# Performance work log

Measured on AMD Instinct MI355X. Metric: run time of the kernel, lower is better.

## Reference

```python
import jax, jax.numpy as jnp
from jax import lax
import numpy as np
import math

H = 768
INNER = 1152  # int(1.5*768), divisible by num_heads
NH = 8
DH = INNER // NH
K = 4
B = 2
S = 2048


def setup_inputs() -> dict:
    key = jax.random.key(0)
    ks = jax.random.split(key, 12)
    sc = 0.02
    inp = {
        'x': jax.random.normal(ks[0], (B, S, H), dtype=jnp.float32),
        'W_up': jax.random.normal(ks[1], (H, 2 * INNER), dtype=jnp.float32) * sc,
        'conv_w': jax.random.normal(ks[2], (INNER, 1, K), dtype=jnp.float32) * sc,  # depthwise OIW
        'conv_b': jnp.zeros((INNER,), dtype=jnp.float32),
        'Wq': jax.random.normal(ks[3], (INNER, INNER), dtype=jnp.float32) * sc,
        'Wk': jax.random.normal(ks[4], (INNER, INNER), dtype=jnp.float32) * sc,
        'Wv': jax.random.normal(ks[5], (INNER, INNER), dtype=jnp.float32) * sc,
        'Wi': jnp.zeros((3 * INNER, NH), dtype=jnp.float32),
        'bi': jax.random.normal(ks[6], (NH,), dtype=jnp.float32) * 0.1,
        'Wf': jnp.zeros((3 * INNER, NH), dtype=jnp.float32),
        'bf': jnp.linspace(3.0, 6.0, NH, dtype=jnp.float32),
        'norm_w': jnp.ones((INNER,), dtype=jnp.float32),
        'skip': jnp.ones((), dtype=jnp.float32),
        'W_down': jax.random.normal(ks[7], (INNER, H), dtype=jnp.float32) * sc,
    }
    return inp


def _multihead_layernorm(h, norm_w, eps=1e-5):
    # per-head layernorm, no bias, computed in fp32
    b, s, d = h.shape
    hh = h.reshape(b, s, NH, DH).astype(jnp.float32)
    mean = hh.mean(axis=-1, keepdims=True)
    var = ((hh - mean) ** 2).mean(axis=-1, keepdims=True)
    hn = (hh - mean) / jnp.sqrt(var + eps)
    return hn.reshape(b, s, d).astype(h.dtype) * norm_w


def _mlstm_cell(q, k, v, Wi, bi, Wf, bf, norm_w):
    b, s, d = q.shape
    eps = 1e-6
    qkv_cat = jnp.concatenate([q, k, v], axis=-1)          # (B,S,3*INNER)
    ig = qkv_cat @ Wi + bi                                  # (B,S,NH)
    fg = qkv_cat @ Wf + bf                                  # (B,S,NH)
    # to (B,NH,S,DH)
    qh = q.reshape(b, s, NH, DH).transpose(0, 2, 1, 3)
    kh = k.reshape(b, s, NH, DH).transpose(0, 2, 1, 3)
    vh = v.reshape(b, s, NH, DH).transpose(0, 2, 1, 3)
    ig = ig.transpose(0, 2, 1)                              # (B,NH,S)
    fg = fg.transpose(0, 2, 1)                              # (B,NH,S)

    log_f = jax.nn.log_sigmoid(fg)                          # (B,NH,S)
    lf_cs = jnp.concatenate([jnp.zeros((b, NH, 1), log_f.dtype),
                             jnp.cumsum(log_f, axis=-1)], axis=-1)  # (B,NH,S+1)
    # entry (i,j) = sum log f_{j+1..i}
    log_fg_mat = lf_cs[:, :, 1:, None] - lf_cs[:, :, None, 1:]      # (B,NH,S,S)
    ltr = jnp.tril(jnp.ones((s, s), dtype=bool))
    log_fg_mat = jnp.where(ltr, log_fg_mat, -jnp.inf)
    log_D = log_fg_mat + ig[:, :, None, :]                  # add igate along columns
    max_log_D = lax.stop_gradient(jnp.max(log_D, axis=-1, keepdims=True))
    D = jnp.exp(log_D - max_log_D)                          # (B,NH,S,S)

    qk = jnp.einsum('bhsd,bhtd->bhst', qh, kh / math.sqrt(DH))
    C = qk * D
    normalizer = jnp.maximum(jnp.abs(C.sum(axis=-1, keepdims=True)),
                             jnp.exp(-max_log_D)) + eps
    h = jnp.einsum('bhst,bhtd->bhsd', C / normalizer, vh)
    h = h.transpose(0, 2, 1, 3).reshape(b, s, d)
    return _multihead_layernorm(h, norm_w)


def reference(x, W_up, conv_w, conv_b, Wq, Wk, Wv, Wi, bi, Wf, bf, norm_w, skip, W_down):
    xz = x @ W_up                                           # (B,S,2*INNER)
    x_mlstm, z = jnp.split(xz, 2, axis=-1)
    # causal depthwise conv1d
    xc = x_mlstm.transpose(0, 2, 1)                         # NCW
    xc = jnp.pad(xc, ((0, 0), (0, 0), (K - 1, 0)))
    xc = lax.conv_general_dilated(xc, conv_w, (1,), 'VALID',
                                  dimension_numbers=('NCW', 'OIW', 'NCW'),
                                  feature_group_count=INNER)
    xc = (xc + conv_b[None, :, None]).transpose(0, 2, 1)    # (B,S,INNER)
    x_conv = jax.nn.silu(xc)
    q = x_conv @ Wq
    k = x_conv @ Wk
    v = x_mlstm @ Wv
    h = _mlstm_cell(q, k, v, Wi, bi, Wf, bf, norm_w)
    h = h + skip * x_conv
    h = h * jax.nn.silu(z)
    return h @ W_down
```

## Files before the change

### kernel.cpp

```cpp
#include <hip/hip_runtime.h>
#include <hip/hip_bf16.h>
#include <math.h>

#define HDIM   768
#define INNER  1152
#define NHEADS 8
#define DHEAD  144
#define SEQ    2048
#define BATCH  2
#define TOKENS (BATCH*SEQ)

using bf16x8 = __attribute__((ext_vector_type(8))) short;
using u16x8  = __attribute__((ext_vector_type(8))) unsigned short;
using f32x4  = __attribute__((ext_vector_type(4))) float;

__device__ __forceinline__ float silu_f(float x) { return x / (1.f + expf(-x)); }

__device__ __forceinline__ unsigned short f2bf(float f) {
    unsigned u = __float_as_uint(f);
    unsigned r = (u + 0x7fffu + ((u >> 16) & 1u)) >> 16;
    return (unsigned short)r;
}
__device__ __forceinline__ float bf2f(unsigned short s) {
    return __uint_as_float(((unsigned)s) << 16);
}

#define MF(a, b, c) __builtin_amdgcn_mfma_f32_16x16x32_bf16(a, b, c, 0, 0, 0)

__global__ __launch_bounds__(256) void convert_act(
    const float* __restrict__ X, int ldx, int Kd, unsigned short* __restrict__ Y) {
    int t = blockIdx.x * 256 + threadIdx.x;
    int kc = Kd >> 3;
    int k8 = t % kc;
    int row = t / kc;
    int k = k8 * 8;
    const float* src = X + (size_t)row * ldx + k;
    float4 v0 = *(const float4*)src;
    float4 v1 = *(const float4*)(src + 4);
    float a[8] = {v0.x, v0.y, v0.z, v0.w, v1.x, v1.y, v1.z, v1.w};
    u16x8 hi, lo;
#pragma unroll
    for (int j = 0; j < 8; ++j) {
        unsigned short h = f2bf(a[j]);
        hi[j] = h;
        lo[j] = f2bf(a[j] - bf2f(h));
    }
    int rb = row >> 7, r = row & 127, kb = k >> 5, c = k & 31;
    int KB = Kd >> 5;
    size_t base = ((size_t)(rb * KB + kb) * 2) * 4096;
    *(u16x8*)&Y[base + r * 32 + c] = hi;
    *(u16x8*)&Y[base + 4096 + r * 32 + c] = lo;
}

__global__ __launch_bounds__(256) void convert_wgt(
    const float* __restrict__ W, int N, int Kd, unsigned short* __restrict__ Y) {
    __shared__ float ls[32][133];
    const int tid = threadIdx.x;
    const int cb = blockIdx.x, kb = blockIdx.y;
    for (int i = tid; i < 4096; i += 256) {
        int kk = i >> 7, n = i & 127;
        ls[kk][n] = W[(size_t)(kb * 32 + kk) * N + cb * 128 + n];
    }
    __syncthreads();
    int KB = Kd >> 5;
    unsigned short* dst = Y + ((size_t)(cb * KB + kb) * 2) * 4096;
#pragma unroll
    for (int g = 0; g < 2; ++g) {
        int u = g * 256 + tid;
        int j = u >> 2, kk0 = (u & 3) * 8;
        u16x8 hi, lo;
#pragma unroll
        for (int e = 0; e < 8; ++e) {
            float a = ls[kk0 + e][j];
            unsigned short h = f2bf(a);
            hi[e] = h;
            lo[e] = f2bf(a - bf2f(h));
        }
        *(u16x8*)&dst[j * 32 + kk0] = hi;
        *(u16x8*)&dst[4096 + j * 32 + kk0] = lo;
    }
}

__global__ __launch_bounds__(256) void gemm_bf16x3(
    const unsigned short* __restrict__ At, const unsigned short* __restrict__ Bt,
    float* __restrict__ C, int N, int KB) {
    __shared__ unsigned short lsA[2][128][32];
    __shared__ unsigned short lsB[2][128][32];
    const int tid = threadIdx.x;
    const int w = tid >> 6, lane = tid & 63;
    const int wr = w >> 1, wc = w & 1;
    const int bx = blockIdx.x, by = blockIdx.y;

    const unsigned short* ga0 = At + ((size_t)by * KB) * 8192;
    const unsigned short* gb0 = Bt + ((size_t)bx * KB) * 8192;
    unsigned short* lsAf = &lsA[0][0][0];
    unsigned short* lsBf = &lsB[0][0][0];

    f32x4 acc[4][4];
#pragma unroll
    for (int i = 0; i < 4; ++i)
#pragma unroll
        for (int j = 0; j < 4; ++j) acc[i][j] = (f32x4){0.f, 0.f, 0.f, 0.f};

    const int kseg = (lane >> 4) * 8;
    const int rl = lane & 15;

    for (int kb = 0; kb < KB; ++kb) {
        __syncthreads();
        const unsigned short* ga = ga0 + (size_t)kb * 8192;
        const unsigned short* gb = gb0 + (size_t)kb * 8192;
#pragma unroll
        for (int p = 0; p < 4; ++p) {
            int chunk = p * 4 + w;
            __builtin_amdgcn_global_load_lds(
                (const __attribute__((address_space(1))) void*)(ga + chunk * 512 + lane * 8),
                (__attribute__((address_space(3))) void*)(lsAf + chunk * 512), 16, 0, 0);
            __builtin_amdgcn_global_load_lds(
                (const __attribute__((address_space(1))) void*)(gb + chunk * 512 + lane * 8),
                (__attribute__((address_space(3))) void*)(lsBf + chunk * 512), 16, 0, 0);
        }
        __syncthreads();

        bf16x8 ah[4], al[4], bh[4], bl[4];
#pragma unroll
        for (int f = 0; f < 4; ++f) {
            ah[f] = *(const bf16x8*)&lsA[0][wr * 64 + f * 16 + rl][kseg];
            al[f] = *(const bf16x8*)&lsA[1][wr * 64 + f * 16 + rl][kseg];
            bh[f] = *(const bf16x8*)&lsB[0][wc * 64 + f * 16 + rl][kseg];
            bl[f] = *(const bf16x8*)&lsB[1][wc * 64 + f * 16 + rl][kseg];
        }
#pragma unroll
        for (int i = 0; i < 4; ++i)
#pragma unroll
            for (int j = 0; j < 4; ++j) {
                acc[i][j] = MF(ah[i], bh[j], acc[i][j]);
                acc[i][j] = MF(ah[i], bl[j], acc[i][j]);
                acc[i][j] = MF(al[i], bh[j], acc[i][j]);
            }
    }

    const int cl = lane & 15, rseg = (lane >> 4) * 4;
#pragma unroll
    for (int i = 0; i < 4; ++i)
#pragma unroll
        for (int j = 0; j < 4; ++j)
#pragma unroll
            for (int r = 0; r < 4; ++r)
                C[(size_t)(by * 128 + wr * 64 + i * 16 + rseg + r) * N +
                  bx * 128 + wc * 64 + j * 16 + cl] = acc[i][j][r];
}

__global__ __launch_bounds__(256) void conv_silu_cvt(
    const float* __restrict__ xz, const float* __restrict__ cw,
    const float* __restrict__ cb, float* __restrict__ xconv,
    unsigned short* __restrict__ ct) {
    int t = blockIdx.x * 256 + threadIdx.x;
    int c8 = t % 144;
    int row = t / 144;
    int c = c8 * 8;
    int s = row & (SEQ - 1);
    float acc[8];
#pragma unroll
    for (int j = 0; j < 8; ++j) acc[j] = cb[c + j];
#pragma unroll
    for (int tap = 0; tap < 4; ++tap) {
        int ss = s - 3 + tap;
        if (ss < 0) continue;
        const float* src = xz + (size_t)(row - 3 + tap) * (2 * INNER) + c;
        float4 v0 = *(const float4*)src;
        float4 v1 = *(const float4*)(src + 4);
        float vv[8] = {v0.x, v0.y, v0.z, v0.w, v1.x, v1.y, v1.z, v1.w};
#pragma unroll
        for (int j = 0; j < 8; ++j) acc[j] += vv[j] * cw[(c + j) * 4 + tap];
    }
    float xc[8];
    u16x8 hi, lo;
#pragma unroll
    for (int j = 0; j < 8; ++j) {
        xc[j] = silu_f(acc[j]);
        unsigned short h = f2bf(xc[j]);
        hi[j] = h;
        lo[j] = f2bf(xc[j] - bf2f(h));
    }
    float4 o0 = {xc[0], xc[1], xc[2], xc[3]};
    float4 o1 = {xc[4], xc[5], xc[6], xc[7]};
    *(float4*)&xconv[(size_t)row * INNER + c] = o0;
    *(float4*)&xconv[(size_t)row * INNER + c + 4] = o1;
    int rb = row >> 7, r = row & 127, kb = c >> 5, cc = c & 31;
    size_t base = ((size_t)(rb * 36 + kb) * 2) * 4096;
    *(u16x8*)&ct[base + r * 32 + cc] = hi;
    *(u16x8*)&ct[base + 4096 + r * 32 + cc] = lo;
}

__global__ __launch_bounds__(256) void gates_kernel(
    const float* __restrict__ qb, const float* __restrict__ kb,
    const float* __restrict__ vb, const float* __restrict__ Wi,
    const float* __restrict__ bi, const float* __restrict__ Wf,
    const float* __restrict__ bf, float* __restrict__ ig, float* __restrict__ logf) {
    __shared__ float red[16][257];
    const int tok = blockIdx.x;
    const int tid = threadIdx.x;
    float aI[8], aF[8];
#pragma unroll
    for (int h = 0; h < 8; ++h) { aI[h] = 0.f; aF[h] = 0.f; }
    const size_t rb = (size_t)tok * INNER;
    for (int d = tid; d < INNER; d += 256) {
        float qv = qb[rb + d], kv = kb[rb + d], vv = vb[rb + d];
        float4 wq0 = *(const float4*)&Wi[(size_t)d * 8];
        float4 wq1 = *(const float4*)&Wi[(size_t)d * 8 + 4];
        float4 wk0 = *(const float4*)&Wi[(size_t)(INNER + d) * 8];
        float4 wk1 = *(const float4*)&Wi[(size_t)(INNER + d) * 8 + 4];
        float4 wv0 = *(const float4*)&Wi[(size_t)(2 * INNER + d) * 8];
        float4 wv1 = *(const float4*)&Wi[(size_t)(2 * INNER + d) * 8 + 4];
        aI[0] += qv * wq0.x + kv * wk0.x + vv * wv0.x;
        aI[1] += qv * wq0.y + kv * wk0.y + vv * wv0.y;
        aI[2] += qv * wq0.z + kv * wk0.z + vv * wv0.z;
        aI[3] += qv * wq0.w + kv * wk0.w + vv * wv0.w;
        aI[4] += qv * wq1.x + kv * wk1.x + vv * wv1.x;
        aI[5] += qv * wq1.y + kv * wk1.y + vv * wv1.y;
        aI[6] += qv * wq1.z + kv * wk1.z + vv * wv1.z;
        aI[7] += qv * wq1.w + kv * wk1.w + vv * wv1.w;
        float4 fq0 = *(const float4*)&Wf[(size_t)d * 8];
        float4 fq1 = *(const float4*)&Wf[(size_t)d * 8 + 4];
        float4 fk0 = *(const float4*)&Wf[(size_t)(INNER + d) * 8];
        float4 fk1 = *(const float4*)&Wf[(size_t)(INNER + d) * 8 + 4];
        float4 fv0 = *(const float4*)&Wf[(size_t)(2 * INNER + d) * 8];
        float4 fv1 = *(const float4*)&Wf[(size_t)(2 * INNER + d) * 8 + 4];
        aF[0] += qv * fq0.x + kv * fk0.x + vv * fv0.x;
        aF[1] += qv * fq0.y + kv * fk0.y + vv * fv0.y;
        aF[2] += qv * fq0.z + kv * fk0.z + vv * fv0.z;
        aF[3] += qv * fq0.w + kv * fk0.w + vv * fv0.w;
        aF[4] += qv * fq1.x + kv * fk1.x + vv * fv1.x;
        aF[5] += qv * fq1.y + kv * fk1.y + vv * fv1.y;
        aF[6] += qv * fq1.z + kv * fk1.z + vv * fv1.z;
        aF[7] += qv * fq1.w + kv * fk1.w + vv * fv1.w;
    }
#pragma unroll
    for (int h = 0; h < 8; ++h) { red[h][tid] = aI[h]; red[8 + h][tid] = aF[h]; }
    __syncthreads();
    for (int off = 128; off > 0; off >>= 1) {
        if (tid < off) {
#pragma unroll
            for (int h = 0; h < 16; ++h) red[h][tid] += red[h][tid + off];
        }
        __syncthreads();
    }
    if (tid < 8) {
        int h = tid;
        int b = tok / SEQ, s = tok % SEQ;
        size_t gidx = (size_t)(b * NHEADS + h) * SEQ + s;
        ig[gidx] = red[h][0] + bi[h];
        float fgv = red[8 + h][0] + bf[h];
        float lf = fminf(fgv, 0.f) - log1pf(expf(-fabsf(fgv)));
        logf[gidx] = lf;
    }
}

__global__ __launch_bounds__(256) void scan_gates(
    float* __restrict__ csb, const float* __restrict__ igb,
    float* __restrict__ ejg, float* __restrict__ pmg) {
    __shared__ float ts[256];
    const int tid = threadIdx.x;
    const size_t base = (size_t)blockIdx.x * SEQ;
    float v[8];
    float run = 0.f;
#pragma unroll
    for (int j = 0; j < 8; ++j) { run += csb[base + tid * 8 + j]; v[j] = run; }
    ts[tid] = run;
    __syncthreads();
    for (int off = 1; off < 256; off <<= 1) {
        float add = (tid >= off) ? ts[tid - off] : 0.f;
        __syncthreads();
        ts[tid] += add;
        __syncthreads();
    }
    float excl = (tid > 0) ? ts[tid - 1] : 0.f;
    float e[8];
#pragma unroll
    for (int j = 0; j < 8; ++j) {
        float c = v[j] + excl;
        csb[base + tid * 8 + j] = c;
        e[j] = igb[base + tid * 8 + j] - c;
        ejg[base + tid * 8 + j] = e[j];
    }
    __syncthreads();
    float m = -INFINITY;
    float pmv[8];
#pragma unroll
    for (int j = 0; j < 8; ++j) { m = fmaxf(m, e[j]); pmv[j] = m; }
    ts[tid] = m;
    __syncthreads();
    for (int off = 1; off < 256; off <<= 1) {
        float mm = (tid >= off) ? ts[tid - off] : -INFINITY;
        __syncthreads();
        ts[tid] = fmaxf(ts[tid], mm);
        __syncthreads();
    }
    float exm = (tid > 0) ? ts[tid - 1] : -INFINITY;
#pragma unroll
    for (int j = 0; j < 8; ++j) pmg[base + tid * 8 + j] = fmaxf(pmv[j], exm);
}

#define DP 160

__global__ __launch_bounds__(256) void qk_convert(
    const float* __restrict__ qb, const float* __restrict__ kb,
    unsigned short* __restrict__ qh, unsigned short* __restrict__ kh) {
    int t = blockIdx.x * 256 + threadIdx.x;
    int seg = t % 20;
    int rest = t / 20;
    int h = rest & 7;
    int token = rest >> 3;
    int b = token >> 11, s = token & (SEQ - 1);
    int bh = b * 8 + h;
    int d0 = seg * 8;
    u16x8 qhi = {0,0,0,0,0,0,0,0}, qlo = qhi, khi = qhi, klo = qhi;
    if (d0 < DHEAD) {
        const float* qs = qb + (size_t)token * INNER + h * DHEAD + d0;
        const float* ks = kb + (size_t)token * INNER + h * DHEAD + d0;
        float4 a0 = *(const float4*)qs, a1 = *(const float4*)(qs + 4);
        float4 b0 = *(const float4*)ks, b1 = *(const float4*)(ks + 4);
        float qa[8] = {a0.x, a0.y, a0.z, a0.w, a1.x, a1.y, a1.z, a1.w};
        float ka[8] = {b0.x, b0.y, b0.z, b0.w, b1.x, b1.y, b1.z, b1.w};
#pragma unroll
        for (int j = 0; j < 8; ++j) {
            unsigned short hq = f2bf(qa[j]);
            qhi[j] = hq;
            qlo[j] = f2bf(qa[j] - bf2f(hq));
            float kv = ka[j] * (1.f / 12.f);
            unsigned short hk = f2bf(kv);
            khi[j] = hk;
            klo[j] = f2bf(kv - bf2f(hk));
        }
    }
    size_t hi_idx = ((size_t)(bh * 2) * SEQ + s) * DP + d0;
    size_t plane = (size_t)SEQ * DP;
    *(u16x8*)&qh[hi_idx] = qhi;
    *(u16x8*)&qh[hi_idx + plane] = qlo;
    *(u16x8*)&kh[hi_idx] = khi;
    *(u16x8*)&kh[hi_idx + plane] = klo;
}

__global__ __launch_bounds__(256) void v_transpose(
    const float* __restrict__ vb, unsigned short* __restrict__ vt) {
    __shared__ float ls[64][148];
    const int tid = threadIdx.x;
    const int sb = blockIdx.x;
    const int bh = blockIdx.y;
    const int b = bh >> 3, h = bh & 7;
    for (int u = tid; u < 64 * 36; u += 256) {
        int s_ = u / 36, c4 = (u % 36) * 4;
        *(float4*)&ls[s_][c4] =
            *(const float4*)&vb[(size_t)(b * SEQ + sb * 64 + s_) * INNER + h * DHEAD + c4];
    }
    __syncthreads();
    for (int u = tid; u < 1152; u += 256) {
        int dd = u >> 3, sc = u & 7;
        u16x8 hi, lo;
#pragma unroll
        for (int i = 0; i < 8; ++i) {
            float a = ls[sc * 8 + i][dd];
            unsigned short hh = f2bf(a);
            hi[i] = hh;
            lo[i] = f2bf(a - bf2f(hh));
        }
        size_t dst = ((size_t)(bh * 2) * 144 + dd) * SEQ + sb * 64 + sc * 8;
        *(u16x8*)&vt[dst] = hi;
        *(u16x8*)&vt[dst + (size_t)144 * SEQ] = lo;
    }
}

#define LKS 168
#define LVS 40
#define PSTR 40

__global__ __launch_bounds__(256) void mlstm_cell_mfma(
    const unsigned short* __restrict__ qh, const unsigned short* __restrict__ kh,
    const unsigned short* __restrict__ vt, const float* __restrict__ ejg,
    const float* __restrict__ pmg, const float* __restrict__ csg,
    float* __restrict__ hcell) {
    __shared__ unsigned short Ks[2][32][LKS];
    __shared__ unsigned short Vs[2][144][LVS];
    __shared__ unsigned short Pl[2][4][16][PSTR];
    __shared__ float ej_s[32];
    __shared__ float scl_s[4][16];
    __shared__ float nrm_s[4][16];

    const int n = blockIdx.x;
    const int bh = n & 15;
    const int ii = n >> 4;
    const int qt = (ii & 1) ? (31 - (ii >> 1)) : (ii >> 1);
    const int b = bh >> 3, h = bh & 7;
    const int qb0 = qt * 64;
    const int tid = threadIdx.x;
    const int w = tid >> 6, lane = tid & 63;
    const int ql = lane & 15;
    const int ss = lane >> 4;
    const int q = qb0 + w * 16 + ql;
    const int gb = bh * SEQ;

    bf16x8 qf[2][5];
#pragma unroll
    for (int l = 0; l < 2; ++l) {
        size_t qbase = ((size_t)(bh * 2 + l) * SEQ + q) * DP;
#pragma unroll
        for (int ks = 0; ks < 5; ++ks)
            qf[l][ks] = *(const bf16x8*)&qh[qbase + ks * 32 + ss * 8];
    }

    f32x4 o[9];
#pragma unroll
    for (int j = 0; j < 9; ++j) o[j] = (f32x4){0.f, 0.f, 0.f, 0.f};
    float ssum = 0.f;
    float pm_run = -INFINITY;
    const int ntiles = 2 * (qt + 1);
    const int wlimit = (qb0 + w * 16 + 15) >> 5;

    for (int t = 0; t < ntiles; ++t) {
        const int kvb = t * 32;
        __syncthreads();
        for (int c = tid; c < 1280; c += 256) {
            int l = c / 640, rem = c % 640, row = rem / 20, seg = rem % 20;
            u16x8 vv = *(const u16x8*)&kh[((size_t)(bh * 2 + l) * SEQ + kvb + row) * DP + seg * 8];
            *(u16x8*)&Ks[l][row][seg * 8] = vv;
        }
        for (int c = tid; c < 1152; c += 256) {
            int l = c / 576, rem = c % 576, dd = rem / 4, seg = rem % 4;
            u16x8 vv = *(const u16x8*)&vt[((size_t)(bh * 2 + l) * 144 + dd) * SEQ + kvb + seg * 8];
            *(u16x8*)&Vs[l][dd][seg * 8] = vv;
        }
        if (tid < 32) ej_s[tid] = ejg[gb + kvb + tid];
        __syncthreads();

        const bool active = (t <= wlimit);
        if (active) {
            const int eq = min(q, kvb + 31);
            const float pm_e = pmg[gb + eq];
            const float sc = __expf(pm_run - pm_e);
            pm_run = pm_e;
            scl_s[w][ql] = sc;

            f32x4 s0 = {0.f, 0.f, 0.f, 0.f}, s1 = s0;
#pragma unroll
            for (int ks = 0; ks < 5; ++ks) {
                bf16x8 a0h = *(const bf16x8*)&Ks[0][ql][ks * 32 + ss * 8];
                bf16x8 a0l = *(const bf16x8*)&Ks[1][ql][ks * 32 + ss * 8];
                bf16x8 a1h = *(const bf16x8*)&Ks[0][16 + ql][ks * 32 + ss * 8];
                bf16x8 a1l = *(const bf16x8*)&Ks[1][16 + ql][ks * 32 + ss * 8];
                s0 = MF(a0h, qf[0][ks], s0);
                s0 = MF(a0h, qf[1][ks], s0);
                s0 = MF(a0l, qf[0][ks], s0);
                s1 = MF(a1h, qf[0][ks], s1);
                s1 = MF(a1h, qf[1][ks], s1);
                s1 = MF(a1l, qf[0][ks], s1);
            }
            float lsum = 0.f;
            float pq[2][4];
#pragma unroll
            for (int f = 0; f < 2; ++f) {
#pragma unroll
                for (int r = 0; r < 4; ++r) {
                    int kv = kvb + f * 16 + 4 * ss + r;
                    float sv = f ? s1[r] : s0[r];
                    float wgt = (kv <= q) ? __expf(ej_s[f * 16 + 4 * ss + r] - pm_e) : 0.f;
                    float p = sv * wgt;
                    pq[f][r] = p;
                    lsum += p;
                }
            }
            ssum = ssum * sc + lsum;
#pragma unroll
            for (int f = 0; f < 2; ++f) {
                unsigned short h0 = f2bf(pq[f][0]), h1 = f2bf(pq[f][1]);
                unsigned short h2 = f2bf(pq[f][2]), h3 = f2bf(pq[f][3]);
                unsigned hi01 = (unsigned)h0 | ((unsigned)h1 << 16);
                unsigned hi23 = (unsigned)h2 | ((unsigned)h3 << 16);
                unsigned short l0 = f2bf(pq[f][0] - bf2f(h0)), l1 = f2bf(pq[f][1] - bf2f(h1));
                unsigned short l2 = f2bf(pq[f][2] - bf2f(h2)), l3 = f2bf(pq[f][3] - bf2f(h3));
                unsigned lo01 = (unsigned)l0 | ((unsigned)l1 << 16);
                unsigned lo23 = (unsigned)l2 | ((unsigned)l3 << 16);
                uint2 hv = {hi01, hi23}, lv = {lo01, lo23};
                *(uint2*)&Pl[0][w][ql][4 * ss + 16 * f] = hv;
                *(uint2*)&Pl[1][w][ql][4 * ss + 16 * f] = lv;
            }
        }
        __syncthreads();
        if (active) {
            bf16x8 ph = *(const bf16x8*)&Pl[0][w][ql][ss * 8];
            bf16x8 pl = *(const bf16x8*)&Pl[1][w][ql][ss * 8];
            float scr[4];
#pragma unroll
            for (int r = 0; r < 4; ++r) scr[r] = scl_s[w][4 * ss + r];
#pragma unroll
            for (int j = 0; j < 9; ++j) {
                f32x4 tacc = o[j];
                tacc[0] *= scr[0]; tacc[1] *= scr[1];
                tacc[2] *= scr[2]; tacc[3] *= scr[3];
                bf16x8 vh = *(const bf16x8*)&Vs[0][16 * j + ql][ss * 8];
                bf16x8 vl = *(const bf16x8*)&Vs[1][16 * j + ql][ss * 8];
                tacc = MF(ph, vh, tacc);
                tacc = MF(pl, vh, tacc);
                tacc = MF(ph, vl, tacc);
                o[j] = tacc;
            }
        }
    }

    ssum += __shfl_xor(ssum, 16);
    ssum += __shfl_xor(ssum, 32);
    float m = csg[gb + q] + pm_run;
    float nrm = fmaxf(fabsf(ssum), __expf(-m)) + 1e-6f;
    nrm_s[w][ql] = 1.f / nrm;
    __syncthreads();
    float invr[4];
#pragma unroll
    for (int r = 0; r < 4; ++r) invr[r] = nrm_s[w][4 * ss + r];
    const size_t hb = ((size_t)(b * SEQ + qb0 + w * 16)) * INNER + h * DHEAD;
#pragma unroll
    for (int j = 0; j < 9; ++j)
#pragma unroll
        for (int r = 0; r < 4; ++r)
            hcell[hb + (size_t)(4 * ss + r) * INNER + 16 * j + ql] = o[j][r] * invr[r];
}

__global__ __launch_bounds__(256) void ln_gate(
    const float* __restrict__ hcell, const float* __restrict__ xconv,
    const float* __restrict__ xz, const float* __restrict__ norm_w,
    const float* __restrict__ skip, float* __restrict__ g) {
    const int unit = blockIdx.x * 4 + (threadIdx.x >> 6);
    const int lane = threadIdx.x & 63;
    const int token = unit >> 3;
    const int h = unit & 7;
    const size_t base = (size_t)token * INNER + h * DHEAD;

    float x0 = hcell[base + lane];
    float x1 = hcell[base + 64 + lane];
    float x2 = (lane < 16) ? hcell[base + 128 + lane] : 0.f;
    float s = x0 + x1 + x2;
#pragma unroll
    for (int off = 32; off > 0; off >>= 1) s += __shfl_down(s, off);
    s = __shfl(s, 0);
    float mean = s * (1.f / 144.f);
    float d0 = x0 - mean, d1 = x1 - mean, d2 = (lane < 16) ? x2 - mean : 0.f;
    float vsum = d0 * d0 + d1 * d1 + d2 * d2;
#pragma unroll
    for (int off = 32; off > 0; off >>= 1) vsum += __shfl_down(vsum, off);
    vsum = __shfl(vsum, 0);
    float rstd = rsqrtf(vsum * (1.f / 144.f) + 1e-5f);
    float sk = skip[0];
    const size_t zbase = (size_t)token * (2 * INNER) + INNER + h * DHEAD;

    {
        float hn = d0 * rstd * norm_w[h * DHEAD + lane];
        g[base + lane] = (hn + sk * xconv[base + lane]) * silu_f(xz[zbase + lane]);
    }
    {
        float hn = d1 * rstd * norm_w[h * DHEAD + 64 + lane];
        g[base + 64 + lane] = (hn + sk * xconv[base + 64 + lane]) * silu_f(xz[zbase + 64 + lane]);
    }
    if (lane < 16) {
        float hn = d2 * rstd * norm_w[h * DHEAD + 128 + lane];
        g[base + 128 + lane] = (hn + sk * xconv[base + 128 + lane]) * silu_f(xz[zbase + 128 + lane]);
    }
}

extern "C" void kernel_launch(void* const* d_in, const int* in_sizes, int n_in,
                              void* d_out, int out_size, void* d_ws, size_t ws_size,
                              hipStream_t stream) {
    const float* x      = (const float*)d_in[0];
    const float* W_up   = (const float*)d_in[1];
    const float* conv_w = (const float*)d_in[2];
    const float* conv_b = (const float*)d_in[3];
    const float* Wq     = (const float*)d_in[4];
    const float* Wk     = (const float*)d_in[5];
    const float* Wv     = (const float*)d_in[6];
    const float* Wi     = (const float*)d_in[7];
    const float* bi     = (const float*)d_in[8];
    const float* Wf     = (const float*)d_in[9];
    const float* bf     = (const float*)d_in[10];
    const float* norm_w = (const float*)d_in[11];
    const float* skip   = (const float*)d_in[12];
    const float* W_down = (const float*)d_in[13];
    float* out = (float*)d_out;

    float* f = (float*)d_ws;
    float* xz    = f; f += 9437184;
    float* xconv = f; f += 4718592;
    float* qb    = f; f += 4718592;
    float* kbuf  = f; f += 4718592;
    float* vb    = f; f += 4718592;
    float* hcell = f; f += 4718592;
    float* igb   = f; f += 32768;
    float* csb   = f; f += 32768;
    float* ejg   = f; f += 32768;
    float* pmg   = f; f += 32768;
    float* regA = f; f += 7864320;
    unsigned short* xh  = (unsigned short*)regA;
    unsigned short* ch  = (unsigned short*)(regA + 3145728);
    unsigned short* kht = (unsigned short*)regA;
    unsigned short* gh  = (unsigned short*)(regA + 3145728);
    float* regB = f; f += 4718592;
    unsigned short* mh  = (unsigned short*)regB;
    unsigned short* vtt = (unsigned short*)regB;
    float* regC = f; f += 5750784;
    unsigned short* wup = (unsigned short*)regC;
    unsigned short* wqt = (unsigned short*)(regC + 1769472);
    unsigned short* wkt = (unsigned short*)(regC + 3096576);
    unsigned short* wvt = (unsigned short*)(regC + 4423680);
    unsigned short* qht = (unsigned short*)regC;
    float* wdtf = f; f += 884736;
    unsigned short* wdt = (unsigned short*)wdtf;

    dim3 blk(256);

    convert_wgt<<<dim3(18, 24), blk, 0, stream>>>(W_up, 2304, 768, wup);
    convert_wgt<<<dim3(9, 36), blk, 0, stream>>>(Wq, 1152, 1152, wqt);
    convert_wgt<<<dim3(9, 36), blk, 0, stream>>>(Wk, 1152, 1152, wkt);
    convert_wgt<<<dim3(9, 36), blk, 0, stream>>>(Wv, 1152, 1152, wvt);
    convert_wgt<<<dim3(6, 36), blk, 0, stream>>>(W_down, 768, 1152, wdt);

    convert_act<<<1536, blk, 0, stream>>>(x, HDIM, HDIM, xh);
    gemm_bf16x3<<<dim3(18, 32), blk, 0, stream>>>(xh, wup, xz, 2304, 24);

    conv_silu_cvt<<<2304, blk, 0, stream>>>(xz, conv_w, conv_b, xconv, ch);
    convert_act<<<2304, blk, 0, stream>>>(xz, 2 * INNER, INNER, mh);

    gemm_bf16x3<<<dim3(9, 32), blk, 0, stream>>>(ch, wqt, qb, INNER, 36);
    gemm_bf16x3<<<dim3(9, 32), blk, 0, stream>>>(ch, wkt, kbuf, INNER, 36);
    gemm_bf16x3<<<dim3(9, 32), blk, 0, stream>>>(mh, wvt, vb, INNER, 36);

    gates_kernel<<<TOKENS, blk, 0, stream>>>(qb, kbuf, vb, Wi, bi, Wf, bf, igb, csb);
    scan_gates<<<BATCH * NHEADS, blk, 0, stream>>>(csb, igb, ejg, pmg);

    qk_convert<<<2560, blk, 0, stream>>>(qb, kbuf, qht, kht);
    v_transpose<<<dim3(32, 16), blk, 0, stream>>>(vb, vtt);
    mlstm_cell_mfma<<<512, blk, 0, stream>>>(qht, kht, vtt, ejg, pmg, csb, hcell);

    ln_gate<<<TOKENS * NHEADS / 4, blk, 0, stream>>>(hcell, xconv, xz, norm_w, skip, qb);
    convert_act<<<2304, blk, 0, stream>>>(qb, INNER, INNER, gh);
    gemm_bf16x3<<<dim3(6, 32), blk, 0, stream>>>(gh, wdt, out, HDIM, 36);
}
```

Baseline: 825.9 us.

## Register-prefetch next K/V tile, drop padding and redundant barriers in mLSTM cell

The mLSTM attention kernel now loads the next K/V/ej tile from global memory into registers while the current tile is computed, then stores them to LDS at the top of the next iteration. This overlaps global-load latency with MFMA work. Precomputed per-thread offsets replace the per-iteration index math. The intra-tile and final __syncthreads are removed, relying on each wave only reading its own Pl/scl/nrm slices. LDS padding is dropped, which risks bank conflicts, and launch bounds now request 3 blocks per CU, which adds register pressure from the prefetch buffers.

```diff
diff --git a/kernel.cpp b/kernel.cpp
--- a/kernel.cpp
+++ b/kernel.cpp
@@ -370,18 +370,14 @@
     }
 }
 
-#define LKS 168
-#define LVS 40
-#define PSTR 40
-
-__global__ __launch_bounds__(256) void mlstm_cell_mfma(
+__global__ __launch_bounds__(256, 3) void mlstm_cell_mfma(
     const unsigned short* __restrict__ qh, const unsigned short* __restrict__ kh,
     const unsigned short* __restrict__ vt, const float* __restrict__ ejg,
     const float* __restrict__ pmg, const float* __restrict__ csg,
     float* __restrict__ hcell) {
-    __shared__ unsigned short Ks[2][32][LKS];
-    __shared__ unsigned short Vs[2][144][LVS];
-    __shared__ unsigned short Pl[2][4][16][PSTR];
+    __shared__ unsigned short Ks[2][32][160];
+    __shared__ unsigned short Vs[2][144][32];
+    __shared__ unsigned short Pl[2][4][16][32];
     __shared__ float ej_s[32];
     __shared__ float scl_s[4][16];
     __shared__ float nrm_s[4][16];
@@ -399,6 +395,27 @@
     const int q = qb0 + w * 16 + ql;
     const int gb = bh * SEQ;
 
+    unsigned goffK[5];
+    unsigned short* ldstK[5];
+#pragma unroll
+    for (int i = 0; i < 5; ++i) {
+        int c = tid + 256 * i;
+        int l = c / 640, rem = c % 640, row = rem / 20, seg = rem % 20;
+        goffK[i] = ((unsigned)(bh * 2 + l) * SEQ + row) * DP + seg * 8;
+        ldstK[i] = &Ks[l][row][seg * 8];
+    }
+    unsigned goffV[5];
+    unsigned short* ldstV[5];
+    const bool v4ok = (tid < 128);
+#pragma unroll
+    for (int i = 0; i < 5; ++i) {
+        int c = tid + 256 * i;
+        int cc = (c < 1152) ? c : 0;
+        int l = cc / 576, rem = cc % 576, dd = rem / 4, seg = rem % 4;
+        goffV[i] = ((unsigned)(bh * 2 + l) * 144 + dd) * SEQ + seg * 8;
+        ldstV[i] = &Vs[l][dd][seg * 8];
+    }
+
     bf16x8 qf[2][5];
 #pragma unroll
     for (int l = 0; l < 2; ++l) {
@@ -416,20 +433,33 @@
     const int ntiles = 2 * (qt + 1);
     const int wlimit = (qb0 + w * 16 + 15) >> 5;
 
+    u16x8 sk[5], sv[5];
+    float ejr = 0.f;
+#pragma unroll
+    for (int i = 0; i < 5; ++i) sk[i] = *(const u16x8*)(kh + goffK[i]);
+#pragma unroll
+    for (int i = 0; i < 5; ++i)
+        if (i < 4 || v4ok) sv[i] = *(const u16x8*)(vt + goffV[i]);
+    if (tid < 32) ejr = ejg[gb + tid];
+
     for (int t = 0; t < ntiles; ++t) {
         const int kvb = t * 32;
         __syncthreads();
-        for (int c = tid; c < 1280; c += 256) {
-            int l = c / 640, rem = c % 640, row = rem / 20, seg = rem % 20;
-            u16x8 vv = *(const u16x8*)&kh[((size_t)(bh * 2 + l) * SEQ + kvb + row) * DP + seg * 8];
-            *(u16x8*)&Ks[l][row][seg * 8] = vv;
-        }
-        for (int c = tid; c < 1152; c += 256) {
-            int l = c / 576, rem = c % 576, dd = rem / 4, seg = rem % 4;
-            u16x8 vv = *(const u16x8*)&vt[((size_t)(bh * 2 + l) * 144 + dd) * SEQ + kvb + seg * 8];
-            *(u16x8*)&Vs[l][dd][seg * 8] = vv;
-        }
-        if (tid < 32) ej_s[tid] = ejg[gb + kvb + tid];
+#pragma unroll
+        for (int i = 0; i < 5; ++i) *(u16x8*)ldstK[i] = sk[i];
+#pragma unroll
+        for (int i = 0; i < 5; ++i)
+            if (i < 4 || v4ok) *(u16x8*)ldstV[i] = sv[i];
+        if (tid < 32) ej_s[tid] = ejr;
+        if (t + 1 < ntiles) {
+            const unsigned koff = (unsigned)(kvb + 32) * DP;
+#pragma unroll
+            for (int i = 0; i < 5; ++i) sk[i] = *(const u16x8*)(kh + goffK[i] + koff);
+#pragma unroll
+            for (int i = 0; i < 5; ++i)
+                if (i < 4 || v4ok) sv[i] = *(const u16x8*)(vt + goffV[i] + (unsigned)(kvb + 32));
+            if (tid < 32) ejr = ejg[gb + kvb + 32 + tid];
+        }
         __syncthreads();
 
         const bool active = (t <= wlimit);
@@ -461,9 +491,9 @@
 #pragma unroll
                 for (int r = 0; r < 4; ++r) {
                     int kv = kvb + f * 16 + 4 * ss + r;
-                    float sv = f ? s1[r] : s0[r];
+                    float sv2 = f ? s1[r] : s0[r];
                     float wgt = (kv <= q) ? __expf(ej_s[f * 16 + 4 * ss + r] - pm_e) : 0.f;
-                    float p = sv * wgt;
+                    float p = sv2 * wgt;
                     pq[f][r] = p;
                     lsum += p;
                 }
@@ -483,9 +513,6 @@
                 *(uint2*)&Pl[0][w][ql][4 * ss + 16 * f] = hv;
                 *(uint2*)&Pl[1][w][ql][4 * ss + 16 * f] = lv;
             }
-        }
-        __syncthreads();
-        if (active) {
             bf16x8 ph = *(const bf16x8*)&Pl[0][w][ql][ss * 8];
             bf16x8 pl = *(const bf16x8*)&Pl[1][w][ql][ss * 8];
             float scr[4];
@@ -511,7 +538,6 @@
     float m = csg[gb + q] + pm_run;
     float nrm = fmaxf(fabsf(ssum), __expf(-m)) + 1e-6f;
     nrm_s[w][ql] = 1.f / nrm;
-    __syncthreads();
     float invr[4];
 #pragma unroll
     for (int r = 0; r < 4; ++r) invr[r] = nrm_s[w][4 * ss + r];
```

Result: slower. 852.8 us (+3.3%).
